# Performance work log

Measured on AMD Instinct MI355X. Metric: run time of the kernel, lower is better.

Reference implementation:

```python
import jax, jax.numpy as jnp
import numpy as np

N_NODES = 100_000
N_EDGES = 1_600_000
IN_DIM = 128          # 2 * in_channels
CONV_OUT = 4          # hard-coded self.conv_out
HID = 64              # hidden_channels
EDIM = 16             # edge_attr_dim
N_STEPS = 8           # fixed-step RK4 over t in [0, 1]
NEG_SLOPE = 0.2       # GATConv default LeakyReLU slope


def setup_inputs() -> dict:
    key = jax.random.key(0)
    ks = jax.random.split(key, 12)

    def lin_w(k, fan_in, fan_out):
        s = 1.0 / np.sqrt(fan_in)
        return jax.random.uniform(k, (fan_in, fan_out), jnp.float32, -s, s)

    x = jax.random.normal(ks[0], (N_NODES, IN_DIM), jnp.float32)
    edge_index = jax.random.randint(ks[1], (2, N_EDGES), 0, N_NODES, dtype=jnp.int64)
    edge_attr = jax.random.normal(ks[2], (N_EDGES, EDIM), jnp.float32)

    W_gat = lin_w(ks[3], IN_DIM, CONV_OUT)
    a_src = jax.random.normal(ks[4], (CONV_OUT,), jnp.float32) * 0.1
    a_dst = jax.random.normal(ks[5], (CONV_OUT,), jnp.float32) * 0.1
    b_gat = jnp.zeros((CONV_OUT,), jnp.float32)

    W1 = lin_w(ks[6], 2 * CONV_OUT + EDIM, HID); b1 = jnp.zeros((HID,), jnp.float32)
    W2 = lin_w(ks[7], HID, HID);                 b2 = jnp.zeros((HID,), jnp.float32)
    W3 = lin_w(ks[8], HID, EDIM);                b3 = jnp.zeros((EDIM,), jnp.float32)

    return dict(x=x, edge_index=edge_index, edge_attr=edge_attr,
                W_gat=W_gat, a_src=a_src, a_dst=a_dst, b_gat=b_gat,
                W1=W1, b1=b1, W2=W2, b2=b2, W3=W3, b3=b3)


def _gat_conv(x, row, col, W_gat, a_src, a_dst, b_gat):
    # single-head PyG GATConv with self-loops, softmax over incoming edges
    loop = jnp.arange(N_NODES)
    r = jnp.concatenate([row, loop])   # source
    c = jnp.concatenate([col, loop])   # destination (aggregation segment)
    h = x @ W_gat                      # [N, CONV_OUT]
    e = jax.nn.leaky_relu((h @ a_src)[r] + (h @ a_dst)[c], NEG_SLOPE)  # [E+N]
    m = jax.ops.segment_max(e, c, num_segments=N_NODES)
    p = jnp.exp(e - m[c])
    denom = jax.ops.segment_sum(p, c, num_segments=N_NODES)
    alpha = p / denom[c]
    out = jax.ops.segment_sum(h[r] * alpha[:, None], c, num_segments=N_NODES)
    return out + b_gat                 # [N, CONV_OUT]


def reference(x, edge_index, edge_attr, W_gat, a_src, a_dst, b_gat,
              W1, b1, W2, b2, W3, b3):
    row, col = edge_index[0], edge_index[1]
    xg = _gat_conv(x, row, col, W_gat, a_src, a_dst, b_gat)
    src = xg[row]   # [E, CONV_OUT]
    tgt = xg[col]   # [E, CONV_OUT]

    def rhs(ea):  # gather-concat-3-layer-MLP, autonomous in t
        f = jnp.concatenate([src, tgt, ea], axis=-1)          # [E, 2*4+EDIM]
        hdd = jax.nn.relu(f @ W1 + b1)
        hdd = jax.nn.relu(hdd @ W2 + b2)
        return hdd @ W3 + b3                                  # [E, EDIM]

    dt = 1.0 / N_STEPS
    def step(ea, _):
        k1 = rhs(ea)
        k2 = rhs(ea + 0.5 * dt * k1)
        k3 = rhs(ea + 0.5 * dt * k2)
        k4 = rhs(ea + dt * k3)
        return ea + (dt / 6.0) * (k1 + 2.0 * k2 + 2.0 * k3 + k4), None

    ea, _ = jax.lax.scan(step, edge_attr, None, length=N_STEPS)
    return ea
```

## Files before the change

### kernel.cpp

```cpp
#include <hip/hip_runtime.h>
#include <math.h>
#include <stdint.h>

#define NN 100000
#define NE 1600000
#define IN_DIM 128
#define HID 64
#define EDIM 16
#define NEG_SLOPE 0.2f

#define OFF_H    0
#define OFF_HS   400000
#define OFF_HD   500000
#define OFF_DEN  600000
#define OFF_XG   700000
#define OFF_IMG  2800000

typedef __attribute__((ext_vector_type(8))) short bf16x8;
typedef __attribute__((ext_vector_type(4))) float f32x4;
typedef __attribute__((ext_vector_type(2))) float f32x2;
typedef __attribute__((ext_vector_type(2))) __bf16 bf16x2;
typedef __attribute__((ext_vector_type(2))) short s16x2;

#define MFMA16(A, B, C) __builtin_amdgcn_mfma_f32_16x16x32_bf16((A), (B), (C), 0, 0, 0)

__device__ inline bf16x8 as_bf(uint4 x) { union { uint4 a; bf16x8 b; } u; u.a = x; return u.b; }
__device__ inline f32x4 as_f4(uint4 x) { union { uint4 a; f32x4 f; } u; u.a = x; return u.f; }

__device__ inline uint32_t pk2(float lo, float hi) {
    f32x2 v; v.x = lo; v.y = hi;
    bf16x2 b = __builtin_convertvector(v, bf16x2);
    union { bf16x2 b; uint32_t u; } uu; uu.b = b; return uu.u;
}

__device__ inline uint32_t pk2r(float lo, float hi) {
    f32x2 v; v.x = lo; v.y = hi;
    bf16x2 b = __builtin_convertvector(v, bf16x2);
    union { bf16x2 b; s16x2 s; uint32_t u; } uu; uu.b = b;
    s16x2 z = {0, 0};
    uu.s = __builtin_elementwise_max(uu.s, z);
    return uu.u;
}

__device__ inline uint16_t f2bf_rne(float f) {
    uint32_t x = __float_as_uint(f);
    uint32_t r = x + 0x7FFFu + ((x >> 16) & 1u);
    return (uint16_t)(r >> 16);
}
__device__ inline uint32_t pk2c(float lo, float hi) {
    return (uint32_t)f2bf_rne(lo) | ((uint32_t)f2bf_rne(hi) << 16);
}

__global__ void node_kernel(const float* __restrict__ x, const float* __restrict__ Wg,
                            const float* __restrict__ a_src, const float* __restrict__ a_dst,
                            float* __restrict__ h, float* __restrict__ hs,
                            float* __restrict__ hd, float* __restrict__ den,
                            float* __restrict__ xg) {
    int i = blockIdx.x * blockDim.x + threadIdx.x;
    if (i >= NN) return;
    float acc0 = 0.f, acc1 = 0.f, acc2 = 0.f, acc3 = 0.f;
    const float* xr = x + (size_t)i * IN_DIM;
#pragma unroll
    for (int d = 0; d < IN_DIM; d += 4) {
        float4 xv = *(const float4*)(xr + d);
        acc0 = fmaf(xv.x, Wg[(d + 0) * 4 + 0], acc0);
        acc1 = fmaf(xv.x, Wg[(d + 0) * 4 + 1], acc1);
        acc2 = fmaf(xv.x, Wg[(d + 0) * 4 + 2], acc2);
        acc3 = fmaf(xv.x, Wg[(d + 0) * 4 + 3], acc3);
        acc0 = fmaf(xv.y, Wg[(d + 1) * 4 + 0], acc0);
        acc1 = fmaf(xv.y, Wg[(d + 1) * 4 + 1], acc1);
        acc2 = fmaf(xv.y, Wg[(d + 1) * 4 + 2], acc2);
        acc3 = fmaf(xv.y, Wg[(d + 1) * 4 + 3], acc3);
        acc0 = fmaf(xv.z, Wg[(d + 2) * 4 + 0], acc0);
        acc1 = fmaf(xv.z, Wg[(d + 2) * 4 + 1], acc1);
        acc2 = fmaf(xv.z, Wg[(d + 2) * 4 + 2], acc2);
        acc3 = fmaf(xv.z, Wg[(d + 2) * 4 + 3], acc3);
        acc0 = fmaf(xv.w, Wg[(d + 3) * 4 + 0], acc0);
        acc1 = fmaf(xv.w, Wg[(d + 3) * 4 + 1], acc1);
        acc2 = fmaf(xv.w, Wg[(d + 3) * 4 + 2], acc2);
        acc3 = fmaf(xv.w, Wg[(d + 3) * 4 + 3], acc3);
    }
    *(float4*)(h + (size_t)i * 4) = make_float4(acc0, acc1, acc2, acc3);
    hs[i] = acc0 * a_src[0] + acc1 * a_src[1] + acc2 * a_src[2] + acc3 * a_src[3];
    hd[i] = acc0 * a_dst[0] + acc1 * a_dst[1] + acc2 * a_dst[2] + acc3 * a_dst[3];
    den[i] = 0.f;
    *(float4*)(xg + (size_t)i * 4) = make_float4(0.f, 0.f, 0.f, 0.f);
}

__global__ void edge_kernel(const int* __restrict__ ei, const float* __restrict__ hs,
                            const float* __restrict__ hd, const float* __restrict__ h,
                            float* __restrict__ den, float* __restrict__ xg) {
    int e = blockIdx.x * blockDim.x + threadIdx.x;
    if (e >= NE) return;
    int r = ei[e], c = ei[NE + e];
    float v = hs[r] + hd[c];
    v = (v >= 0.f) ? v : NEG_SLOPE * v;
    float pe = expf(v);
    float4 hv = *(const float4*)(h + (size_t)r * 4);
    atomicAdd(&den[c], pe);
    atomicAdd(&xg[4 * c + 0], pe * hv.x);
    atomicAdd(&xg[4 * c + 1], pe * hv.y);
    atomicAdd(&xg[4 * c + 2], pe * hv.z);
    atomicAdd(&xg[4 * c + 3], pe * hv.w);
}

__global__ void div_kernel(const float* __restrict__ hs, const float* __restrict__ hd,
                           const float* __restrict__ h, float* __restrict__ xg,
                           const float* __restrict__ den, const float* __restrict__ b_gat) {
    int i = blockIdx.x * blockDim.x + threadIdx.x;
    if (i >= NN) return;
    float v = hs[i] + hd[i];
    v = (v >= 0.f) ? v : NEG_SLOPE * v;
    float pe = expf(v);
    float4 hv = *(const float4*)(h + (size_t)i * 4);
    float inv = 1.0f / (den[i] + pe);
    float4 n = *(const float4*)(xg + (size_t)i * 4);
    *(float4*)(xg + (size_t)i * 4) =
        make_float4(fmaf(fmaf(pe, hv.x, n.x), inv, b_gat[0]),
                    fmaf(fmaf(pe, hv.y, n.y), inv, b_gat[1]),
                    fmaf(fmaf(pe, hv.z, n.z), inv, b_gat[2]),
                    fmaf(fmaf(pe, hv.w, n.w), inv, b_gat[3]));
}

__global__ void prep_kernel(const float* __restrict__ W1, const float* __restrict__ b1,
                            const float* __restrict__ W2, const float* __restrict__ b2,
                            const float* __restrict__ W3, const float* __restrict__ b3,
                            uint32_t* __restrict__ img) {
    int l = threadIdx.x;
    if (l >= 64) return;
    int e = l & 15, g = l >> 4;
    int er = e & 3, eq = e >> 2;
    for (int q = 0; q < 4; ++q) {
        int u = 32 * (q & 1) + 8 * eq + 4 * (q >> 1) + er;
        img[q * 256 + l * 4 + 0] = pk2c(W1[(8 + 4 * g + 0) * 64 + u], W1[(8 + 4 * g + 1) * 64 + u]);
        img[q * 256 + l * 4 + 1] = pk2c(W1[(8 + 4 * g + 2) * 64 + u], W1[(8 + 4 * g + 3) * 64 + u]);
        img[q * 256 + l * 4 + 2] = pk2c(W1[(2 * g + 0) * 64 + u], W1[(2 * g + 1) * 64 + u]);
        img[q * 256 + l * 4 + 3] = pk2c((g == 0) ? b1[u] : 0.f, 0.f);
    }
    for (int t = 0; t < 2; ++t)
        for (int q = 0; q < 4; ++q) {
            int u = 32 * (q & 1) + 8 * eq + 4 * (q >> 1) + er;
            for (int j2 = 0; j2 < 4; ++j2) {
                int k0 = 32 * t + 8 * g + 2 * j2;
                img[(4 + t * 4 + q) * 256 + l * 4 + j2] =
                    pk2c(W2[k0 * 64 + u], W2[(k0 + 1) * 64 + u]);
            }
        }
    for (int t = 0; t < 2; ++t)
        for (int j2 = 0; j2 < 4; ++j2) {
            int k0 = 32 * t + 8 * g + 2 * j2;
            img[(12 + t) * 256 + l * 4 + j2] =
                pk2c(W3[k0 * 16 + e], W3[(k0 + 1) * 16 + e]);
        }
    for (int q = 0; q < 4; ++q)
        for (int r = 0; r < 4; ++r)
            img[(14 + q) * 256 + l * 4 + r] =
                __float_as_uint(b2[32 * (q & 1) + 8 * g + 4 * (q >> 1) + r]);
    for (int r = 0; r < 4; ++r)
        img[18 * 256 + l * 4 + r] = __float_as_uint(b3[4 * g + r]);
}

__global__ __launch_bounds__(256, 4) void rk4_kernel(
    const int* __restrict__ ei, const float* __restrict__ ea,
    const float* __restrict__ xg, const uint32_t* __restrict__ img,
    float* __restrict__ out) {
    const int tid = threadIdx.x;
    const int w = tid >> 6, l = tid & 63;
    const int e = l & 15, g = l >> 4;
    const int edge = blockIdx.x * 64 + w * 16 + e;

    uint4 F[19];
#pragma unroll
    for (int i = 0; i < 19; ++i) F[i] = *(const uint4*)(img + i * 256 + l * 4);

    const bf16x8 W1f0 = as_bf(F[0]), W1f1 = as_bf(F[1]), W1f2 = as_bf(F[2]), W1f3 = as_bf(F[3]);
    const bf16x8 W2f00 = as_bf(F[4]), W2f01 = as_bf(F[5]), W2f02 = as_bf(F[6]), W2f03 = as_bf(F[7]);
    const bf16x8 W2f10 = as_bf(F[8]), W2f11 = as_bf(F[9]), W2f12 = as_bf(F[10]), W2f13 = as_bf(F[11]);
    const bf16x8 W3f0 = as_bf(F[12]), W3f1 = as_bf(F[13]);
    const f32x4 b2f0 = as_f4(F[14]), b2f1 = as_f4(F[15]), b2f2 = as_f4(F[16]), b2f3 = as_f4(F[17]);
    const f32x4 b3f = as_f4(F[18]);

    uint32_t Stf, Stb;
    {
        int idx = (g < 2) ? ei[edge] : ei[NE + edge];
        const float2 fv = *(const float2*)(xg + (size_t)idx * 4 + ((2 * g) & 3));
        Stf = pk2(fv.x, fv.y);
        Stb = (g == 0) ? 0x00003F80u : 0u;
    }

    float4 y4 = *(const float4*)(ea + (size_t)edge * 16 + 4 * g);
    float yv0 = y4.x, yv1 = y4.y, yv2 = y4.z, yv3 = y4.w;

    const f32x4 zero4 = {0.f, 0.f, 0.f, 0.f};
    const float dt6 = 0.125f / 6.0f;

    auto rhs = [&](float a0, float a1, float a2, float a3) -> f32x4 {
        uint4 bb;
        bb.x = pk2(a0, a1); bb.y = pk2(a2, a3); bb.z = Stf; bb.w = Stb;
        bf16x8 B1 = as_bf(bb);
        __builtin_amdgcn_s_setprio(1);
        f32x4 h0 = MFMA16(W1f0, B1, zero4);
        f32x4 h1 = MFMA16(W1f1, B1, zero4);
        f32x4 h2 = MFMA16(W1f2, B1, zero4);
        f32x4 h3 = MFMA16(W1f3, B1, zero4);
        uint4 q20, q21;
        q20.x = pk2r(h0[0], h0[1]);
        q20.y = pk2r(h0[2], h0[3]);
        q20.z = pk2r(h2[0], h2[1]);
        q20.w = pk2r(h2[2], h2[3]);
        q21.x = pk2r(h1[0], h1[1]);
        q21.y = pk2r(h1[2], h1[3]);
        q21.z = pk2r(h3[0], h3[1]);
        q21.w = pk2r(h3[2], h3[3]);
        bf16x8 B20 = as_bf(q20), B21 = as_bf(q21);
        f32x4 p0 = MFMA16(W2f00, B20, b2f0); p0 = MFMA16(W2f10, B21, p0);
        f32x4 p1 = MFMA16(W2f01, B20, b2f1); p1 = MFMA16(W2f11, B21, p1);
        f32x4 p2 = MFMA16(W2f02, B20, b2f2); p2 = MFMA16(W2f12, B21, p2);
        f32x4 p3 = MFMA16(W2f03, B20, b2f3); p3 = MFMA16(W2f13, B21, p3);
        uint4 q30, q31;
        q30.x = pk2r(p0[0], p0[1]);
        q30.y = pk2r(p0[2], p0[3]);
        q30.z = pk2r(p2[0], p2[1]);
        q30.w = pk2r(p2[2], p2[3]);
        q31.x = pk2r(p1[0], p1[1]);
        q31.y = pk2r(p1[2], p1[3]);
        q31.z = pk2r(p3[0], p3[1]);
        q31.w = pk2r(p3[2], p3[3]);
        bf16x8 B30 = as_bf(q30), B31 = as_bf(q31);
        f32x4 kk = MFMA16(W3f0, B30, b3f);
        kk = MFMA16(W3f1, B31, kk);
        __builtin_amdgcn_s_setprio(0);
        return kk;
    };

#pragma unroll 1
    for (int step = 0; step < 8; ++step) {
        float a0 = yv0, a1 = yv1, a2 = yv2, a3 = yv3;
        float c0 = 0.f, c1 = 0.f, c2 = 0.f, c3 = 0.f;
#pragma unroll 1
        for (int s = 0; s < 4; ++s) {
            f32x4 kk = rhs(a0, a1, a2, a3);
            float wk = (s == 1 || s == 2) ? 2.f : 1.f;
            float cs = (s < 2) ? 0.0625f : (s == 2) ? 0.125f : 0.f;
            c0 = fmaf(wk, kk[0], c0); c1 = fmaf(wk, kk[1], c1);
            c2 = fmaf(wk, kk[2], c2); c3 = fmaf(wk, kk[3], c3);
            a0 = fmaf(cs, kk[0], yv0); a1 = fmaf(cs, kk[1], yv1);
            a2 = fmaf(cs, kk[2], yv2); a3 = fmaf(cs, kk[3], yv3);
        }
        yv0 = fmaf(dt6, c0, yv0); yv1 = fmaf(dt6, c1, yv1);
        yv2 = fmaf(dt6, c2, yv2); yv3 = fmaf(dt6, c3, yv3);
    }

    *(float4*)(out + (size_t)edge * 16 + 4 * g) = make_float4(yv0, yv1, yv2, yv3);
}

extern "C" void kernel_launch(void* const* d_in, const int* in_sizes, int n_in,
                              void* d_out, int out_size, void* d_ws, size_t ws_size,
                              hipStream_t stream) {
    const float* x     = (const float*)d_in[0];
    const int*   ei    = (const int*)d_in[1];
    const float* ea    = (const float*)d_in[2];
    const float* Wg    = (const float*)d_in[3];
    const float* a_src = (const float*)d_in[4];
    const float* a_dst = (const float*)d_in[5];
    const float* b_gat = (const float*)d_in[6];
    const float* W1    = (const float*)d_in[7];
    const float* b1    = (const float*)d_in[8];
    const float* W2    = (const float*)d_in[9];
    const float* b2    = (const float*)d_in[10];
    const float* W3    = (const float*)d_in[11];
    const float* b3    = (const float*)d_in[12];

    float* ws  = (float*)d_ws;
    float* h   = ws + OFF_H;
    float* hs  = ws + OFF_HS;
    float* hd  = ws + OFF_HD;
    float* den = ws + OFF_DEN;
    float* xg  = ws + OFF_XG;
    uint32_t* img = (uint32_t*)(ws + OFF_IMG);

    prep_kernel<<<1, 64, 0, stream>>>(W1, b1, W2, b2, W3, b3, img);
    node_kernel<<<(NN + 255) / 256, 256, 0, stream>>>(x, Wg, a_src, a_dst,
                                                      h, hs, hd, den, xg);
    edge_kernel<<<NE / 256, 256, 0, stream>>>(ei, hs, hd, h, den, xg);
    div_kernel<<<(NN + 255) / 256, 256, 0, stream>>>(hs, hd, h, xg, den, b_gat);
    rk4_kernel<<<NE / 64, 256, 0, stream>>>(ei, ea, xg, img, (float*)d_out);
}
```

Baseline: 936.5 us.

## Split dependent MFMA chains and process two edges per thread in edge kernel

In the RK4 MLP, each pair of dependent MFMAs that accumulated into one register is replaced by two independent MFMAs whose results are summed with VALU adds. The intent is to shorten the MFMA dependency chain so the issue latency is hidden. The edge scatter kernel now handles two edges per thread with int2 index loads and half the grid, and uses fast __expf in the edge and div kernels. The costs are extra VALU adds and registers, plus slightly different rounding.

```diff
diff --git a/kernel.cpp b/kernel.cpp
--- a/kernel.cpp
+++ b/kernel.cpp
@@ -87,21 +87,32 @@
     *(float4*)(xg + (size_t)i * 4) = make_float4(0.f, 0.f, 0.f, 0.f);
 }
 
-__global__ void edge_kernel(const int* __restrict__ ei, const float* __restrict__ hs,
-                            const float* __restrict__ hd, const float* __restrict__ h,
-                            float* __restrict__ den, float* __restrict__ xg) {
-    int e = blockIdx.x * blockDim.x + threadIdx.x;
+__global__ __launch_bounds__(256) void edge_kernel(
+    const int* __restrict__ ei, const float* __restrict__ hs,
+    const float* __restrict__ hd, const float* __restrict__ h,
+    float* __restrict__ den, float* __restrict__ xg) {
+    int t = blockIdx.x * blockDim.x + threadIdx.x;
+    int e = 2 * t;
     if (e >= NE) return;
-    int r = ei[e], c = ei[NE + e];
-    float v = hs[r] + hd[c];
-    v = (v >= 0.f) ? v : NEG_SLOPE * v;
-    float pe = expf(v);
-    float4 hv = *(const float4*)(h + (size_t)r * 4);
-    atomicAdd(&den[c], pe);
-    atomicAdd(&xg[4 * c + 0], pe * hv.x);
-    atomicAdd(&xg[4 * c + 1], pe * hv.y);
-    atomicAdd(&xg[4 * c + 2], pe * hv.z);
-    atomicAdd(&xg[4 * c + 3], pe * hv.w);
+    int2 rr = *(const int2*)(ei + e);
+    int2 cc = *(const int2*)(ei + NE + e);
+    float v0 = hs[rr.x] + hd[cc.x];
+    float v1 = hs[rr.y] + hd[cc.y];
+    v0 = (v0 >= 0.f) ? v0 : NEG_SLOPE * v0;
+    v1 = (v1 >= 0.f) ? v1 : NEG_SLOPE * v1;
+    float p0 = __expf(v0), p1 = __expf(v1);
+    float4 h0 = *(const float4*)(h + (size_t)rr.x * 4);
+    float4 h1 = *(const float4*)(h + (size_t)rr.y * 4);
+    atomicAdd(&den[cc.x], p0);
+    atomicAdd(&xg[4 * cc.x + 0], p0 * h0.x);
+    atomicAdd(&xg[4 * cc.x + 1], p0 * h0.y);
+    atomicAdd(&xg[4 * cc.x + 2], p0 * h0.z);
+    atomicAdd(&xg[4 * cc.x + 3], p0 * h0.w);
+    atomicAdd(&den[cc.y], p1);
+    atomicAdd(&xg[4 * cc.y + 0], p1 * h1.x);
+    atomicAdd(&xg[4 * cc.y + 1], p1 * h1.y);
+    atomicAdd(&xg[4 * cc.y + 2], p1 * h1.z);
+    atomicAdd(&xg[4 * cc.y + 3], p1 * h1.w);
 }
 
 __global__ void div_kernel(const float* __restrict__ hs, const float* __restrict__ hd,
@@ -111,7 +122,7 @@
     if (i >= NN) return;
     float v = hs[i] + hd[i];
     v = (v >= 0.f) ? v : NEG_SLOPE * v;
-    float pe = expf(v);
+    float pe = __expf(v);
     float4 hv = *(const float4*)(h + (size_t)i * 4);
     float inv = 1.0f / (den[i] + pe);
     float4 n = *(const float4*)(xg + (size_t)i * 4);
@@ -213,23 +224,28 @@
         q21.z = pk2r(h3[0], h3[1]);
         q21.w = pk2r(h3[2], h3[3]);
         bf16x8 B20 = as_bf(q20), B21 = as_bf(q21);
-        f32x4 p0 = MFMA16(W2f00, B20, b2f0); p0 = MFMA16(W2f10, B21, p0);
-        f32x4 p1 = MFMA16(W2f01, B20, b2f1); p1 = MFMA16(W2f11, B21, p1);
-        f32x4 p2 = MFMA16(W2f02, B20, b2f2); p2 = MFMA16(W2f12, B21, p2);
-        f32x4 p3 = MFMA16(W2f03, B20, b2f3); p3 = MFMA16(W2f13, B21, p3);
+        f32x4 p0 = MFMA16(W2f00, B20, b2f0); f32x4 p0b = MFMA16(W2f10, B21, zero4);
+        f32x4 p1 = MFMA16(W2f01, B20, b2f1); f32x4 p1b = MFMA16(W2f11, B21, zero4);
+        f32x4 p2 = MFMA16(W2f02, B20, b2f2); f32x4 p2b = MFMA16(W2f12, B21, zero4);
+        f32x4 p3 = MFMA16(W2f03, B20, b2f3); f32x4 p3b = MFMA16(W2f13, B21, zero4);
         uint4 q30, q31;
-        q30.x = pk2r(p0[0], p0[1]);
-        q30.y = pk2r(p0[2], p0[3]);
-        q30.z = pk2r(p2[0], p2[1]);
-        q30.w = pk2r(p2[2], p2[3]);
-        q31.x = pk2r(p1[0], p1[1]);
-        q31.y = pk2r(p1[2], p1[3]);
-        q31.z = pk2r(p3[0], p3[1]);
-        q31.w = pk2r(p3[2], p3[3]);
+        q30.x = pk2r(p0[0] + p0b[0], p0[1] + p0b[1]);
+        q30.y = pk2r(p0[2] + p0b[2], p0[3] + p0b[3]);
+        q30.z = pk2r(p2[0] + p2b[0], p2[1] + p2b[1]);
+        q30.w = pk2r(p2[2] + p2b[2], p2[3] + p2b[3]);
+        q31.x = pk2r(p1[0] + p1b[0], p1[1] + p1b[1]);
+        q31.y = pk2r(p1[2] + p1b[2], p1[3] + p1b[3]);
+        q31.z = pk2r(p3[0] + p3b[0], p3[1] + p3b[1]);
+        q31.w = pk2r(p3[2] + p3b[2], p3[3] + p3b[3]);
         bf16x8 B30 = as_bf(q30), B31 = as_bf(q31);
-        f32x4 kk = MFMA16(W3f0, B30, b3f);
-        kk = MFMA16(W3f1, B31, kk);
+        f32x4 ka = MFMA16(W3f0, B30, b3f);
+        f32x4 kb = MFMA16(W3f1, B31, zero4);
         __builtin_amdgcn_s_setprio(0);
+        f32x4 kk;
+        kk[0] = ka[0] + kb[0];
+        kk[1] = ka[1] + kb[1];
+        kk[2] = ka[2] + kb[2];
+        kk[3] = ka[3] + kb[3];
         return kk;
     };
 
@@ -282,7 +298,7 @@
     prep_kernel<<<1, 64, 0, stream>>>(W1, b1, W2, b2, W3, b3, img);
     node_kernel<<<(NN + 255) / 256, 256, 0, stream>>>(x, Wg, a_src, a_dst,
                                                       h, hs, hd, den, xg);
-    edge_kernel<<<NE / 256, 256, 0, stream>>>(ei, hs, hd, h, den, xg);
+    edge_kernel<<<NE / 512, 256, 0, stream>>>(ei, hs, hd, h, den, xg);
     div_kernel<<<(NN + 255) / 256, 256, 0, stream>>>(hs, hd, h, xg, den, b_gat);
     rk4_kernel<<<NE / 64, 256, 0, stream>>>(ei, ea, xg, img, (float*)d_out);
 }
```

New measurement: 1.012 ms. +8.1%, slower.
